# Performance work log

Hardware: AMD Instinct MI355X
Metric: run time of the kernel (lower is better)

Reference implementation:

```python
import jax, jax.numpy as jnp
import numpy as np

NUM_HEADS = 12
DIM_HEAD = 32
EMBED_DIM = NUM_HEADS * DIM_HEAD  # 384
EPS = 1e-5


def _channel_layernorm(x, w, b):
    # LayerNorm over channel axis (axis=1) of [B, D, S, L], per spatial position
    mu = jnp.mean(x, axis=1, keepdims=True)
    var = jnp.mean(jnp.square(x - mu), axis=1, keepdims=True)
    xn = (x - mu) / jnp.sqrt(var + EPS)
    return xn * w[None, :, None, None] + b[None, :, None, None]


def _qkv(x, w, b):
    # 1x1 conv == per-position matmul: [3D, D] x [B, D, S, L] -> [B, 3D, S, L]
    B, D, S, L = x.shape
    y = jnp.einsum('od,bdsl->bosl', w, x) + b[None, :, None, None]
    q, k, v = jnp.split(y, 3, axis=1)
    shp = (B, NUM_HEADS, DIM_HEAD, S, L)
    return q.reshape(shp), k.reshape(shp), v.reshape(shp)


def setup_inputs() -> dict:
    key = jax.random.key(0)
    ks = jax.random.split(key, 5)
    B, D, S, L = 1, EMBED_DIM, 128, 256
    x = jax.random.normal(ks[0], (B, D, S, L), dtype=jnp.float32)
    row_w = jax.random.normal(ks[1], (3 * D, D), dtype=jnp.float32) * (D ** -0.5)
    row_b = jax.random.normal(ks[2], (3 * D,), dtype=jnp.float32) * 0.02
    col_w = jax.random.normal(ks[3], (3 * D, D), dtype=jnp.float32) * (D ** -0.5)
    col_b = jax.random.normal(ks[4], (3 * D,), dtype=jnp.float32) * 0.02
    return {
        'x': x,
        'row_w': row_w, 'row_b': row_b,
        'col_w': col_w, 'col_b': col_b,
        'ln1_w': jnp.ones((D,), jnp.float32), 'ln1_b': jnp.zeros((D,), jnp.float32),
        'ln2_w': jnp.ones((D,), jnp.float32), 'ln2_b': jnp.zeros((D,), jnp.float32),
    }


def reference(x, row_w, row_b, col_w, col_b, ln1_w, ln1_b, ln2_w, ln2_b):
    B, D, S, L = x.shape
    # --- row attention (attend across L within each row s) ---
    q, k, v = _qkv(x, row_w, row_b)  # [B,H,C,S,L]
    row_attn = jnp.einsum('bhcsi,bhcsj->bhsij', q, k)  # note: no 1/sqrt(d) scaling (faithful)
    row_attn = jax.nn.softmax(row_attn, axis=-1)
    row_out = jnp.einsum('bhsij,bhdsj->bhdsi', row_attn, v).reshape(B, D, S, L)
    out = _channel_layernorm(x + row_out, ln1_w, ln1_b)
    # --- column attention (attend across S within each column l) ---
    q, k, v = _qkv(out, col_w, col_b)
    col_attn = jnp.einsum('bhcil,bhcjl->bhijl', q, k)
    col_attn = jax.nn.softmax(col_attn, axis=-2)
    col_out = jnp.einsum('bhijl,bhdjl->bhdil', col_attn, v).reshape(B, D, S, L)
    out = _channel_layernorm(out + col_out, ln2_w, ln2_b)
    return out
```

## Files before the change

### kernel.cpp

```cpp
#include <hip/hip_runtime.h>
#include <math.h>

#define DCH 384
#define NH 12
#define CH 32
#define SS 128
#define LL 256
#define NPOS 32768
#define THREE_D 1152

typedef _Float16 f16_t;
typedef _Float16 f16x4 __attribute__((ext_vector_type(4)));
typedef _Float16 f16x8 __attribute__((ext_vector_type(8)));
typedef float f32x4 __attribute__((ext_vector_type(4)));

#define GLD16(gptr, lptr) __builtin_amdgcn_global_load_lds( \
    (const __attribute__((address_space(1))) unsigned int*)(gptr), \
    (__attribute__((address_space(3))) unsigned int*)(lptr), 16, 0, 0)

#define WAVE_LDS_FENCE() __asm__ volatile("s_waitcnt lgkmcnt(0)" ::: "memory")

__global__ __launch_bounds__(256) void conv_w(const float* __restrict__ in,
                                              f16_t* __restrict__ out, int n4) {
    int i = blockIdx.x * 256 + threadIdx.x;
    if (i < n4) {
        float4 v = ((const float4*)in)[i];
        unsigned short u0 = __builtin_bit_cast(unsigned short, (f16_t)v.x);
        unsigned short u1 = __builtin_bit_cast(unsigned short, (f16_t)v.y);
        unsigned short u2 = __builtin_bit_cast(unsigned short, (f16_t)v.z);
        unsigned short u3 = __builtin_bit_cast(unsigned short, (f16_t)v.w);
        uint2 r;
        r.x = (unsigned)u0 | ((unsigned)u1 << 16);
        r.y = (unsigned)u2 | ((unsigned)u3 << 16);
        ((uint2*)out)[i] = r;
    }
}

__global__ __launch_bounds__(256) void conv_xT(const float* __restrict__ in,
                                               f16_t* __restrict__ outp) {
    __shared__ float tile[64][65];
    const int p0 = blockIdx.x * 64;
    const int k0 = blockIdx.y * 64;
    const int tx = threadIdx.x & 63, ty = threadIdx.x >> 6;
#pragma unroll
    for (int i = 0; i < 16; ++i)
        tile[ty * 16 + i][tx] = in[(size_t)(k0 + ty * 16 + i) * NPOS + p0 + tx];
    __syncthreads();
    const int pr = threadIdx.x >> 2;
    const int cg = threadIdx.x & 3;
    union { uint4 v[2]; unsigned int u[8]; } res;
#pragma unroll
    for (int j = 0; j < 8; ++j) {
        unsigned short lo = __builtin_bit_cast(unsigned short, (f16_t)tile[cg * 16 + 2 * j][pr]);
        unsigned short hi = __builtin_bit_cast(unsigned short, (f16_t)tile[cg * 16 + 2 * j + 1][pr]);
        res.u[j] = (unsigned)lo | ((unsigned)hi << 16);
    }
    uint4* dst = (uint4*)&outp[(size_t)(p0 + pr) * DCH + k0 + cg * 16];
    dst[0] = res.v[0];
    dst[1] = res.v[1];
}

__global__ __launch_bounds__(512) void qkv_gemm_f16(
        const f16_t* __restrict__ Wh,
        const float* __restrict__ bias,
        const f16_t* __restrict__ Xp,
        f16_t* __restrict__ Yq, f16_t* __restrict__ Yk, f16_t* __restrict__ Yv)
{
    __shared__ f16_t sha[128 * 384];
    const int tid  = threadIdx.x;
    const int lane = tid & 63;
    const int wave = tid >> 6;

    const int hwid = blockIdx.y * 9 + blockIdx.x;
    const int nid  = (hwid & 7) * 144 + (hwid >> 3);
    const int ot   = nid % 9;
    const int pt   = nid / 9;
    const int o0 = ot * 128;
    const int p0 = pt * 256;

    const int mrow = lane & 15;
    const int kgq  = lane >> 4;

#pragma unroll
    for (int j = 0; j < 12; ++j) {
        const int ibase = (wave * 12 + j) * 64;
        const int i = ibase + lane;
        const int row = i / 48;
        const int s = i - row * 48;
        const int g = s ^ (row & 7);
        GLD16(Wh + (size_t)(o0 + row) * DCH + g * 8, sha + (size_t)ibase * 8);
    }

    const f16_t* bp0 = Xp + (size_t)(p0 + wave * 32 + mrow) * DCH + kgq * 8;
    const f16_t* bp1 = bp0 + (size_t)16 * DCH;

    f32x4 acc[8][2] = {};
    f16x8 breg[3][2];

    breg[0][0] = *(const f16x8*)(bp0);
    breg[0][1] = *(const f16x8*)(bp1);
    breg[1][0] = *(const f16x8*)(bp0 + 32);
    breg[1][1] = *(const f16x8*)(bp1 + 32);

    __syncthreads();

    const int key = mrow & 7;
    constexpr int NK = DCH / 32;
#pragma unroll
    for (int t = 0; t < NK; ++t) {
        if (t + 2 < NK) {
            breg[(t + 2) % 3][0] = *(const f16x8*)(bp0 + (t + 2) * 32);
            breg[(t + 2) % 3][1] = *(const f16x8*)(bp1 + (t + 2) * 32);
        }
        const int soff = ((t * 4 + kgq) ^ key) * 8;
#pragma unroll
        for (int mi = 0; mi < 8; ++mi) {
            const f16x8 a = *(const f16x8*)(sha + (size_t)(mi * 16 + mrow) * DCH + soff);
            acc[mi][0] = __builtin_amdgcn_mfma_f32_16x16x32_f16(
                a, breg[t % 3][0], acc[mi][0], 0, 0, 0);
            acc[mi][1] = __builtin_amdgcn_mfma_f32_16x16x32_f16(
                a, breg[t % 3][1], acc[mi][1], 0, 0, 0);
        }
    }

    const int col = lane & 15;
    const int rq4 = (lane >> 4) * 4;
    const int qkv = ot / 3;
    const int grp = ot % 3;

    if (qkv < 2) {
        f16_t* Yt = (qkv == 0) ? Yq : Yk;
#pragma unroll
        for (int mi = 0; mi < 8; ++mi) {
            const int h  = grp * 4 + (mi >> 1);
            const int cb = (mi & 1) * 16 + rq4;
            const int ob = o0 + mi * 16 + rq4;
            const float b0 = bias[ob], b1 = bias[ob + 1];
            const float b2 = bias[ob + 2], b3 = bias[ob + 3];
#pragma unroll
            for (int ni = 0; ni < 2; ++ni) {
                const int p = p0 + wave * 32 + ni * 16 + col;
                union { uint2 u; f16_t h4[4]; } w;
                w.h4[0] = (f16_t)(acc[mi][ni][0] + b0);
                w.h4[1] = (f16_t)(acc[mi][ni][1] + b1);
                w.h4[2] = (f16_t)(acc[mi][ni][2] + b2);
                w.h4[3] = (f16_t)(acc[mi][ni][3] + b3);
                *(uint2*)(Yt + ((size_t)h * NPOS + p) * CH + cb) = w.u;
            }
        }
    } else {
#pragma unroll
        for (int mi = 0; mi < 8; ++mi) {
#pragma unroll
            for (int r = 0; r < 4; ++r) {
                const int cg = grp * 128 + mi * 16 + rq4 + r;
                const float br = bias[768 + cg];
#pragma unroll
                for (int ni = 0; ni < 2; ++ni) {
                    const int p = p0 + wave * 32 + ni * 16 + col;
                    Yv[(size_t)cg * NPOS + p] = (f16_t)(acc[mi][ni][r] + br);
                }
            }
        }
    }
}

template <int SEQ, bool XT16>
__global__ __launch_bounds__(256) void mfma_attn(
        const f16_t* __restrict__ Yq, const f16_t* __restrict__ Yk,
        const f16_t* __restrict__ Yv, const void* __restrict__ Xv_,
        float* __restrict__ R)
{
    constexpr int JT  = SEQ / 16;
    constexpr int NIT = SEQ / 64;
    constexpr int PST = SEQ + 8;
    constexpr int VST = SEQ + 8;
    __shared__ f16_t Ks[SEQ * CH];
    __shared__ f16_t Vs[CH * VST];
    __shared__ f16_t pb[4][16 * PST];
    const int tid  = threadIdx.x;
    const int lane = tid & 63;
    const int wave = tid >> 6;
    const int col = lane & 15, quad = lane >> 4;
    const int h = blockIdx.x % NH;
    const size_t pbase = (size_t)(blockIdx.x / NH) * SEQ;

    const f16_t* qg = Yq + ((size_t)h * NPOS + pbase) * CH;
    const f16_t* kg = Yk + ((size_t)h * NPOS + pbase) * CH;
    const f16_t* vg = Yv + (size_t)h * CH * NPOS + pbase;
    f16_t* mypb = pb[wave];

    {
        const int ksw = (lane & 3) ^ ((lane >> 3) & 3);
        const int lrow32 = (lane >> 2) * 32;
#pragma unroll
        for (int i = 0; i < SEQ / 64; ++i) {
            const int off = (wave * (SEQ / 64) + i) * 512;
            GLD16(kg + off + lrow32 + ksw * 8, Ks + off);
        }
    }
    {
        constexpr int CPR = SEQ / 8;
        const int vch = tid % CPR;
        const int vr0 = tid / CPR;
#pragma unroll
        for (int r = vr0; r < CH; r += 256 / CPR)
            *(float4*)(Vs + r * VST + vch * 8) =
                *(const float4*)(vg + (size_t)r * NPOS + vch * 8);
    }
    __syncthreads();

    const int kq8 = (quad ^ ((col >> 1) & 3)) * 8;

    for (int it = 0; it < NIT; ++it) {
        const int i0 = (wave * NIT + it) * 16;
        const f16x8 qf = *(const f16x8*)(qg + (size_t)(i0 + col) * CH + quad * 8);
        f32x4 st[JT];
#pragma unroll
        for (int mt = 0; mt < JT; ++mt) {
            f16x8 kf = *(const f16x8*)(Ks + (mt * 16 + col) * CH + kq8);
            st[mt] = __builtin_amdgcn_mfma_f32_16x16x32_f16(kf, qf, (f32x4){0.f, 0.f, 0.f, 0.f}, 0, 0, 0);
        }
        float sum = 0.f;
#pragma unroll
        for (int mt = 0; mt < JT; ++mt)
#pragma unroll
            for (int r = 0; r < 4; ++r) {
                st[mt][r] = __expf(st[mt][r]);
                sum += st[mt][r];
            }
        sum += __shfl_xor(sum, 16, 64);
        sum += __shfl_xor(sum, 32, 64);
        const float inv = 1.f / sum;
#pragma unroll
        for (int mt = 0; mt < JT; ++mt) {
            union { uint2 u; f16_t h4[4]; } w;
            w.h4[0] = (f16_t)(st[mt][0] * inv);
            w.h4[1] = (f16_t)(st[mt][1] * inv);
            w.h4[2] = (f16_t)(st[mt][2] * inv);
            w.h4[3] = (f16_t)(st[mt][3] * inv);
            *(uint2*)(mypb + col * PST + mt * 16 + quad * 4) = w.u;
        }
        WAVE_LDS_FENCE();

        f32x4 o0a = {0.f, 0.f, 0.f, 0.f}, o0b = {0.f, 0.f, 0.f, 0.f};
        f32x4 o1a = {0.f, 0.f, 0.f, 0.f}, o1b = {0.f, 0.f, 0.f, 0.f};
#pragma unroll
        for (int ks = 0; ks < SEQ / 32; ks += 2) {
            f16x8 pf0 = *(const f16x8*)(mypb + col * PST + ks * 32 + quad * 8);
            f16x8 pf1 = *(const f16x8*)(mypb + col * PST + (ks + 1) * 32 + quad * 8);
            f16x8 va0 = *(const f16x8*)(Vs + col * VST + ks * 32 + quad * 8);
            f16x8 va1 = *(const f16x8*)(Vs + col * VST + (ks + 1) * 32 + quad * 8);
            f16x8 vb0 = *(const f16x8*)(Vs + (16 + col) * VST + ks * 32 + quad * 8);
            f16x8 vb1 = *(const f16x8*)(Vs + (16 + col) * VST + (ks + 1) * 32 + quad * 8);
            o0a = __builtin_amdgcn_mfma_f32_16x16x32_f16(va0, pf0, o0a, 0, 0, 0);
            o0b = __builtin_amdgcn_mfma_f32_16x16x32_f16(va1, pf1, o0b, 0, 0, 0);
            o1a = __builtin_amdgcn_mfma_f32_16x16x32_f16(vb0, pf0, o1a, 0, 0, 0);
            o1b = __builtin_amdgcn_mfma_f32_16x16x32_f16(vb1, pf1, o1b, 0, 0, 0);
        }
        const f32x4 ot0 = o0a + o0b;
        const f32x4 ot1 = o1a + o1b;

        const size_t pos = pbase + i0 + col;
        if constexpr (XT16) {
            const f16_t* Xh = (const f16_t*)Xv_;
            const f16x4 xa = *(const f16x4*)(Xh + pos * DCH + h * CH + quad * 4);
            const f16x4 xb = *(const f16x4*)(Xh + pos * DCH + h * CH + 16 + quad * 4);
#pragma unroll
            for (int r = 0; r < 4; ++r) {
                R[(size_t)(h * CH + quad * 4 + r) * NPOS + pos]      = (float)xa[r] + ot0[r];
                R[(size_t)(h * CH + 16 + quad * 4 + r) * NPOS + pos] = (float)xb[r] + ot1[r];
            }
        } else {
            const float* Xf = (const float*)Xv_;
#pragma unroll
            for (int r = 0; r < 4; ++r) {
                const size_t c0r = (size_t)(h * CH + quad * 4 + r) * NPOS + pos;
                const size_t c1r = (size_t)(h * CH + 16 + quad * 4 + r) * NPOS + pos;
                R[c0r] = Xf[c0r] + ot0[r];
                R[c1r] = Xf[c1r] + ot1[r];
            }
        }
    }
}

__global__ __launch_bounds__(256) void ln_stats(const float* __restrict__ A,
                                                float* __restrict__ mu,
                                                float* __restrict__ rs) {
    __shared__ float ssum[4][64], ssq[4][64];
    const int i = threadIdx.x & 63;
    const int g = threadIdx.x >> 6;
    const int p = blockIdx.x * 64 + i;
    float sum = 0.f, sq = 0.f;
    const float* ap = A + (size_t)(g * 96) * NPOS + p;
#pragma unroll 4
    for (int d = 0; d < 96; ++d) {
        float v = ap[(size_t)d * NPOS];
        sum += v;
        sq += v * v;
    }
    ssum[g][i] = sum;
    ssq[g][i] = sq;
    __syncthreads();
    if (g == 0) {
        float s = ssum[0][i] + ssum[1][i] + ssum[2][i] + ssum[3][i];
        float q = ssq[0][i] + ssq[1][i] + ssq[2][i] + ssq[3][i];
        float m = s * (1.f / DCH);
        float var = q * (1.f / DCH) - m * m;
        mu[p] = m;
        rs[p] = rsqrtf(var + 1e-5f);
    }
}

__global__ __launch_bounds__(256) void norm_xT(
        const float* __restrict__ A, const float* __restrict__ mu,
        const float* __restrict__ rs, const float* __restrict__ w,
        const float* __restrict__ b, f16_t* __restrict__ Xp) {
    __shared__ float tile[64][65];
    const int l0 = (blockIdx.x & 3) * 64;
    const int s  = (blockIdx.x >> 2) & (SS - 1);
    const int k0 = (blockIdx.x >> 9) * 64;
    const int tx = threadIdx.x & 63, ty = threadIdx.x >> 6;
    const int pos0 = s * LL + l0;
#pragma unroll
    for (int i = 0; i < 16; ++i) {
        const int d = k0 + ty * 16 + i;
        float v = A[(size_t)d * NPOS + pos0 + tx];
        tile[ty * 16 + i][tx] = (v - mu[pos0 + tx]) * rs[pos0 + tx] * w[d] + b[d];
    }
    __syncthreads();
    const int pr = threadIdx.x >> 2;
    const int cg = threadIdx.x & 3;
    union { uint4 v[2]; unsigned int u[8]; } res;
#pragma unroll
    for (int j = 0; j < 8; ++j) {
        unsigned short lo = __builtin_bit_cast(unsigned short, (f16_t)tile[cg * 16 + 2 * j][pr]);
        unsigned short hi = __builtin_bit_cast(unsigned short, (f16_t)tile[cg * 16 + 2 * j + 1][pr]);
        res.u[j] = (unsigned)lo | ((unsigned)hi << 16);
    }
    uint4* dst = (uint4*)&Xp[(size_t)((l0 + pr) * SS + s) * DCH + k0 + cg * 16];
    dst[0] = res.v[0];
    dst[1] = res.v[1];
}

__global__ __launch_bounds__(256) void norm_transpose(
        const float* __restrict__ in, const float* __restrict__ mu,
        const float* __restrict__ rs, const float* __restrict__ w,
        const float* __restrict__ b, float* __restrict__ out, int Rr, int Cc) {
    __shared__ float tile[32][33];
    const int ntc = Cc >> 5, ntr = Rr >> 5;
    int tc = blockIdx.x % ntc;
    int tr = (blockIdx.x / ntc) % ntr;
    int d = blockIdx.x / (ntc * ntr);
    int tx = threadIdx.x & 31, ty = threadIdx.x >> 5;
    const float* ip = in + (size_t)d * Rr * Cc;
    float* op = out + (size_t)d * Rr * Cc;
    const float wd = w[d], bd = b[d];
#pragma unroll
    for (int i = 0; i < 32; i += 8) {
        const int r = tr * 32 + ty + i;
        const int c = tc * 32 + tx;
        const int pos = r * Cc + c;
        float v = ip[(size_t)r * Cc + c];
        tile[ty + i][tx] = (v - mu[pos]) * rs[pos] * wd + bd;
    }
    __syncthreads();
#pragma unroll
    for (int i = 0; i < 32; i += 8)
        op[(size_t)(tc * 32 + ty + i) * Rr + tr * 32 + tx] = tile[tx][ty + i];
}

extern "C" void kernel_launch(void* const* d_in, const int* in_sizes, int n_in,
                              void* d_out, int out_size, void* d_ws, size_t ws_size,
                              hipStream_t stream) {
    const float* x     = (const float*)d_in[0];
    const float* row_w = (const float*)d_in[1];
    const float* row_b = (const float*)d_in[2];
    const float* col_w = (const float*)d_in[3];
    const float* col_b = (const float*)d_in[4];
    const float* ln1_w = (const float*)d_in[5];
    const float* ln1_b = (const float*)d_in[6];
    const float* ln2_w = (const float*)d_in[7];
    const float* ln2_b = (const float*)d_in[8];
    float* out = (float*)d_out;

    char* ws = (char*)d_ws;
    const size_t ysz = (size_t)NH * NPOS * CH * 2;
    const size_t abytes = (size_t)DCH * NPOS * 4;
    f16_t* Yq = (f16_t*)ws;
    f16_t* Yk = (f16_t*)(ws + ysz);
    f16_t* Yv = (f16_t*)(ws + 2 * ysz);
    float* A  = (float*)(ws + 3 * ysz);
    f16_t* Xp = (f16_t*)(ws + 3 * ysz + abytes);
    f16_t* Wh = (f16_t*)(ws + 3 * ysz + abytes + ysz);
    float* MU = (float*)(ws + 3 * ysz + abytes + ysz + (1 << 21));
    float* RS = MU + NPOS;

    dim3 ggrid(THREE_D / 128, NPOS / 256);
    const int wn4 = THREE_D * DCH / 4;
    dim3 cgrid(NPOS / 64, DCH / 64);

    conv_w<<<(wn4 + 255) / 256, 256, 0, stream>>>(row_w, Wh, wn4);
    conv_xT<<<cgrid, 256, 0, stream>>>(x, Xp);
    qkv_gemm_f16<<<ggrid, 512, 0, stream>>>(Wh, row_b, Xp, Yq, Yk, Yv);
    mfma_attn<LL, false><<<NH * SS, 256, 0, stream>>>(Yq, Yk, Yv, x, A);
    ln_stats<<<NPOS / 64, 256, 0, stream>>>(A, MU, RS);
    norm_xT<<<(DCH / 64) * SS * (LL / 64), 256, 0, stream>>>(A, MU, RS, ln1_w, ln1_b, Xp);

    conv_w<<<(wn4 + 255) / 256, 256, 0, stream>>>(col_w, Wh, wn4);
    qkv_gemm_f16<<<ggrid, 512, 0, stream>>>(Wh, col_b, Xp, Yq, Yk, Yv);
    mfma_attn<SS, true><<<NH * LL, 256, 0, stream>>>(Yq, Yk, Yv, Xp, A);
    ln_stats<<<NPOS / 64, 256, 0, stream>>>(A, MU, RS);
    norm_transpose<<<DCH * (LL / 32) * (SS / 32), 256, 0, stream>>>(
        A, MU, RS, ln2_w, ln2_b, out, LL, SS);
}
```

Baseline: 342.8 us.

## Fuse LayerNorm statistics into attention epilogue via atomics and store residual in fp16

The attention epilogue now accumulates per-position sum and sum of squares with wave shuffles and atomicAdd into zeroed buffers, which removes the separate ln_stats pass over the residual tensor. The residual tensor A is also stored as fp16 instead of fp32, halving its write and read traffic. The normalize kernels derive mean and rstd from the sums. The cost is 24 atomic contributions per position, extra zeroing launches, reduced precision in the residual, and a one-pass variance formula that can lose precision.

```diff
diff --git a/kernel.cpp b/kernel.cpp
--- a/kernel.cpp
+++ b/kernel.cpp
@@ -36,6 +36,10 @@
     }
 }
 
+__global__ __launch_bounds__(256) void zero_stats(float* __restrict__ p) {
+    ((float4*)p)[blockIdx.x * 256 + threadIdx.x] = (float4){0.f, 0.f, 0.f, 0.f};
+}
+
 __global__ __launch_bounds__(256) void conv_xT(const float* __restrict__ in,
                                                f16_t* __restrict__ outp) {
     __shared__ float tile[64][65];
@@ -169,7 +173,7 @@
 __global__ __launch_bounds__(256) void mfma_attn(
         const f16_t* __restrict__ Yq, const f16_t* __restrict__ Yk,
         const f16_t* __restrict__ Yv, const void* __restrict__ Xv_,
-        float* __restrict__ R)
+        f16_t* __restrict__ R, float* __restrict__ SUM, float* __restrict__ SQ)
 {
     constexpr int JT  = SEQ / 16;
     constexpr int NIT = SEQ / 64;
@@ -262,59 +266,46 @@
         const f32x4 ot1 = o1a + o1b;
 
         const size_t pos = pbase + i0 + col;
+        float a0[4], a1[4];
         if constexpr (XT16) {
             const f16_t* Xh = (const f16_t*)Xv_;
             const f16x4 xa = *(const f16x4*)(Xh + pos * DCH + h * CH + quad * 4);
             const f16x4 xb = *(const f16x4*)(Xh + pos * DCH + h * CH + 16 + quad * 4);
 #pragma unroll
             for (int r = 0; r < 4; ++r) {
-                R[(size_t)(h * CH + quad * 4 + r) * NPOS + pos]      = (float)xa[r] + ot0[r];
-                R[(size_t)(h * CH + 16 + quad * 4 + r) * NPOS + pos] = (float)xb[r] + ot1[r];
+                a0[r] = (float)xa[r] + ot0[r];
+                a1[r] = (float)xb[r] + ot1[r];
             }
         } else {
             const float* Xf = (const float*)Xv_;
 #pragma unroll
             for (int r = 0; r < 4; ++r) {
-                const size_t c0r = (size_t)(h * CH + quad * 4 + r) * NPOS + pos;
-                const size_t c1r = (size_t)(h * CH + 16 + quad * 4 + r) * NPOS + pos;
-                R[c0r] = Xf[c0r] + ot0[r];
-                R[c1r] = Xf[c1r] + ot1[r];
+                a0[r] = Xf[(size_t)(h * CH + quad * 4 + r) * NPOS + pos] + ot0[r];
+                a1[r] = Xf[(size_t)(h * CH + 16 + quad * 4 + r) * NPOS + pos] + ot1[r];
             }
         }
-    }
-}
-
-__global__ __launch_bounds__(256) void ln_stats(const float* __restrict__ A,
-                                                float* __restrict__ mu,
-                                                float* __restrict__ rs) {
-    __shared__ float ssum[4][64], ssq[4][64];
-    const int i = threadIdx.x & 63;
-    const int g = threadIdx.x >> 6;
-    const int p = blockIdx.x * 64 + i;
-    float sum = 0.f, sq = 0.f;
-    const float* ap = A + (size_t)(g * 96) * NPOS + p;
-#pragma unroll 4
-    for (int d = 0; d < 96; ++d) {
-        float v = ap[(size_t)d * NPOS];
-        sum += v;
-        sq += v * v;
-    }
-    ssum[g][i] = sum;
-    ssq[g][i] = sq;
-    __syncthreads();
-    if (g == 0) {
-        float s = ssum[0][i] + ssum[1][i] + ssum[2][i] + ssum[3][i];
-        float q = ssq[0][i] + ssq[1][i] + ssq[2][i] + ssq[3][i];
-        float m = s * (1.f / DCH);
-        float var = q * (1.f / DCH) - m * m;
-        mu[p] = m;
-        rs[p] = rsqrtf(var + 1e-5f);
+        float psum = 0.f, psq = 0.f;
+#pragma unroll
+        for (int r = 0; r < 4; ++r) {
+            R[(size_t)(h * CH + quad * 4 + r) * NPOS + pos]      = (f16_t)a0[r];
+            R[(size_t)(h * CH + 16 + quad * 4 + r) * NPOS + pos] = (f16_t)a1[r];
+            psum += a0[r] + a1[r];
+            psq  += a0[r] * a0[r] + a1[r] * a1[r];
+        }
+        psum += __shfl_xor(psum, 16, 64);
+        psum += __shfl_xor(psum, 32, 64);
+        psq  += __shfl_xor(psq, 16, 64);
+        psq  += __shfl_xor(psq, 32, 64);
+        if (quad == 0) {
+            atomicAdd(&SUM[pos], psum);
+            atomicAdd(&SQ[pos], psq);
+        }
     }
 }
 
 __global__ __launch_bounds__(256) void norm_xT(
-        const float* __restrict__ A, const float* __restrict__ mu,
-        const float* __restrict__ rs, const float* __restrict__ w,
+        const f16_t* __restrict__ A, const float* __restrict__ SUM,
+        const float* __restrict__ SQ, const float* __restrict__ w,
         const float* __restrict__ b, f16_t* __restrict__ Xp) {
     __shared__ float tile[64][65];
     const int l0 = (blockIdx.x & 3) * 64;
@@ -322,11 +313,13 @@
     const int k0 = (blockIdx.x >> 9) * 64;
     const int tx = threadIdx.x & 63, ty = threadIdx.x >> 6;
     const int pos0 = s * LL + l0;
+    const float m  = SUM[pos0 + tx] * (1.f / DCH);
+    const float rs = rsqrtf(SQ[pos0 + tx] * (1.f / DCH) - m * m + 1e-5f);
 #pragma unroll
     for (int i = 0; i < 16; ++i) {
         const int d = k0 + ty * 16 + i;
-        float v = A[(size_t)d * NPOS + pos0 + tx];
-        tile[ty * 16 + i][tx] = (v - mu[pos0 + tx]) * rs[pos0 + tx] * w[d] + b[d];
+        float v = (float)A[(size_t)d * NPOS + pos0 + tx];
+        tile[ty * 16 + i][tx] = (v - m) * rs * w[d] + b[d];
     }
     __syncthreads();
     const int pr = threadIdx.x >> 2;
@@ -344,8 +337,8 @@
 }
 
 __global__ __launch_bounds__(256) void norm_transpose(
-        const float* __restrict__ in, const float* __restrict__ mu,
-        const float* __restrict__ rs, const float* __restrict__ w,
+        const f16_t* __restrict__ in, const float* __restrict__ SUM,
+        const float* __restrict__ SQ, const float* __restrict__ w,
         const float* __restrict__ b, float* __restrict__ out, int Rr, int Cc) {
     __shared__ float tile[32][33];
     const int ntc = Cc >> 5, ntr = Rr >> 5;
@@ -353,7 +346,7 @@
     int tr = (blockIdx.x / ntc) % ntr;
     int d = blockIdx.x / (ntc * ntr);
     int tx = threadIdx.x & 31, ty = threadIdx.x >> 5;
-    const float* ip = in + (size_t)d * Rr * Cc;
+    const f16_t* ip = in + (size_t)d * Rr * Cc;
     float* op = out + (size_t)d * Rr * Cc;
     const float wd = w[d], bd = b[d];
 #pragma unroll
@@ -361,8 +354,10 @@
         const int r = tr * 32 + ty + i;
         const int c = tc * 32 + tx;
         const int pos = r * Cc + c;
-        float v = ip[(size_t)r * Cc + c];
-        tile[ty + i][tx] = (v - mu[pos]) * rs[pos] * wd + bd;
+        const float m  = SUM[pos] * (1.f / DCH);
+        const float rs = rsqrtf(SQ[pos] * (1.f / DCH) - m * m + 1e-5f);
+        float v = (float)ip[(size_t)r * Cc + c];
+        tile[ty + i][tx] = (v - m) * rs * wd + bd;
     }
     __syncthreads();
 #pragma unroll
@@ -390,11 +385,11 @@
     f16_t* Yq = (f16_t*)ws;
     f16_t* Yk = (f16_t*)(ws + ysz);
     f16_t* Yv = (f16_t*)(ws + 2 * ysz);
-    float* A  = (float*)(ws + 3 * ysz);
+    f16_t* A  = (f16_t*)(ws + 3 * ysz);
     f16_t* Xp = (f16_t*)(ws + 3 * ysz + abytes);
     f16_t* Wh = (f16_t*)(ws + 3 * ysz + abytes + ysz);
-    float* MU = (float*)(ws + 3 * ysz + abytes + ysz + (1 << 21));
-    float* RS = MU + NPOS;
+    float* SUMB = (float*)(ws + 3 * ysz + abytes + ysz + (1 << 21));
+    float* SQB  = SUMB + NPOS;
 
     dim3 ggrid(THREE_D / 128, NPOS / 256);
     const int wn4 = THREE_D * DCH / 4;
@@ -402,15 +397,15 @@
 
     conv_w<<<(wn4 + 255) / 256, 256, 0, stream>>>(row_w, Wh, wn4);
     conv_xT<<<cgrid, 256, 0, stream>>>(x, Xp);
+    zero_stats<<<2 * NPOS / 1024, 256, 0, stream>>>(SUMB);
     qkv_gemm_f16<<<ggrid, 512, 0, stream>>>(Wh, row_b, Xp, Yq, Yk, Yv);
-    mfma_attn<LL, false><<<NH * SS, 256, 0, stream>>>(Yq, Yk, Yv, x, A);
-    ln_stats<<<NPOS / 64, 256, 0, stream>>>(A, MU, RS);
-    norm_xT<<<(DCH / 64) * SS * (LL / 64), 256, 0, stream>>>(A, MU, RS, ln1_w, ln1_b, Xp);
+    mfma_attn<LL, false><<<NH * SS, 256, 0, stream>>>(Yq, Yk, Yv, x, A, SUMB, SQB);
+    norm_xT<<<(DCH / 64) * SS * (LL / 64), 256, 0, stream>>>(A, SUMB, SQB, ln1_w, ln1_b, Xp);
 
     conv_w<<<(wn4 + 255) / 256, 256, 0, stream>>>(col_w, Wh, wn4);
+    zero_stats<<<2 * NPOS / 1024, 256, 0, stream>>>(SUMB);
     qkv_gemm_f16<<<ggrid, 512, 0, stream>>>(Wh, col_b, Xp, Yq, Yk, Yv);
-    mfma_attn<SS, true><<<NH * LL, 256, 0, stream>>>(Yq, Yk, Yv, Xp, A);
-    ln_stats<<<NPOS / 64, 256, 0, stream>>>(A, MU, RS);
+    mfma_attn<SS, true><<<NH * LL, 256, 0, stream>>>(Yq, Yk, Yv, Xp, A, SUMB, SQB);
     norm_transpose<<<DCH * (LL / 32) * (SS / 32), 256, 0, stream>>>(
-        A, MU, RS, ln2_w, ln2_b, out, LL, SS);
-}
+        A, SUMB, SQB, ln2_w, ln2_b, out, LL, SS);
+}
```

New measurement: 320.7 us. 6.5% less time.
